# Kernel optimization log

Hardware: AMD Instinct MI355X
Metric: run time of the kernel (lower is better)

## Reference

```python
import jax, jax.numpy as jnp
import numpy as np

N_NODES, IN_DIM, HID, LAT, N_EDGES = 50000, 3000, 512, 30, 800000
NEG_SLOPE = 0.2


def setup_inputs() -> dict:
    key = jax.random.key(0)
    ks = jax.random.split(key, 6)
    x = jax.random.normal(ks[0], (N_NODES, IN_DIM), dtype=jnp.float32)
    edge_index = jax.random.randint(ks[1], (2, N_EDGES), 0, N_NODES, dtype=jnp.int64)
    # xavier-normal-ish scales
    W1 = jax.random.normal(ks[2], (IN_DIM, HID), dtype=jnp.float32) * 0.02
    W2 = jax.random.normal(ks[3], (HID, LAT), dtype=jnp.float32) * 0.06
    att_src = jax.random.normal(ks[4], (HID,), dtype=jnp.float32) * 0.1
    att_dst = jax.random.normal(ks[5], (HID,), dtype=jnp.float32) * 0.1
    return {"x": x, "edge_index": edge_index, "W1": W1, "W2": W2,
            "att_src": att_src, "att_dst": att_dst}


def _segment_softmax(e, seg, num_segments):
    # numerically stable softmax over variable-degree dst neighborhoods
    m = jax.ops.segment_max(e, seg, num_segments=num_segments)
    m = jnp.where(jnp.isfinite(m), m, 0.0)  # empty segments -> 0, harmless
    p = jnp.exp(e - m[seg])
    s = jax.ops.segment_sum(p, seg, num_segments=num_segments)
    return p / (s[seg] + 1e-16)


def reference(x, edge_index, W1, W2, att_src, att_dst):
    N = x.shape[0]
    src, dst = edge_index[0], edge_index[1]  # messages flow src(j) -> dst(i)

    # ---- conv1: full GAT layer (heads=1, no self-loops, no bias) ----
    h1 = x @ W1                                   # [N, 512]
    a_src = h1 @ att_src                          # [N]
    a_dst = h1 @ att_dst                          # [N]
    e = jax.nn.leaky_relu(a_src[src] + a_dst[dst], NEG_SLOPE)  # [E]
    alpha = _segment_softmax(e, dst, N)           # [E] (also tied attn for conv3)
    agg1 = jax.ops.segment_sum(h1[src] * alpha[:, None], dst, num_segments=N)
    x1 = jax.nn.elu(agg1)                         # [N, 512]

    # ---- conv2: attention=False -> plain linear projection ----
    x2 = x1 @ W2                                  # [N, 30] (latent embedding)

    # ---- conv3: tied weights (W2^T) + tied attention from conv1 ----
    h3 = x2 @ W2.T                                # [N, 512]
    agg3 = jax.ops.segment_sum(h3[src] * alpha[:, None], dst, num_segments=N)
    x3 = jax.nn.elu(agg3)

    # ---- conv4: attention=False, tied weights (W1^T) ----
    x4 = x3 @ W1.T                                # [N, in_channels]
    return (x2, x4)
```

## Files before the change

kernel.cpp:

```cpp
#include <hip/hip_runtime.h>

#define N_NODES 50000
#define IN_DIM  3000
#define HID     512
#define LAT     30
#define N_EDGES 800000
#define M_PAD   50048
#define M_PAD2  50176
#define K1_PAD  3008
#define N4_PAD  3072

typedef __bf16 bf16;
typedef unsigned int uint;
typedef __attribute__((ext_vector_type(4))) float f32x4;
typedef __attribute__((ext_vector_type(8))) bf16 bf16x8;

__device__ __forceinline__ float bf2f(bf16 b){ return (float)b; }

__device__ __forceinline__ void gl16(const void* g, void* l){
  __builtin_amdgcn_global_load_lds(
      (const __attribute__((address_space(1))) void*)g,
      (__attribute__((address_space(3))) void*)l, 16, 0, 0);
}

__device__ __forceinline__ int xcd_swz(int orig, int nwg){
  int q = nwg >> 3, r = nwg & 7;
  int xcd = orig & 7, lid = orig >> 3;
  return (xcd < r ? xcd*(q+1) : r*(q+1) + (xcd-r)*q) + lid;
}

__global__ void k_w1t(const float* __restrict__ W1, bf16* __restrict__ W1T){
  int k = blockIdx.x*256 + threadIdx.x;
  int n = blockIdx.y;
  if (k >= K1_PAD) return;
  float v = (k < IN_DIM) ? W1[(long)k*HID + n] : 0.f;
  int kt = k >> 5, c = (k >> 3) & 3, off = k & 7;
  int p = c ^ ((n >> 1) & 3);
  W1T[(long)n*K1_PAD + kt*32 + p*8 + off] = (bf16)v;
}
__global__ void k_w1p(const float* __restrict__ W1, bf16* __restrict__ W1P){
  int k = blockIdx.x*256 + threadIdx.x;
  int n = blockIdx.y;
  if (k >= HID) return;
  float v = (n < IN_DIM) ? W1[(long)n*HID + k] : 0.f;
  int kt = k >> 5, c = (k >> 3) & 3, off = k & 7;
  int p = c ^ ((n >> 1) & 3);
  W1P[(long)n*HID + kt*32 + p*8 + off] = (bf16)v;
}
__global__ void k_w2t(const float* __restrict__ W2, bf16* __restrict__ W2T){
  int k = blockIdx.x*256 + threadIdx.x;
  int n = blockIdx.y;
  if (k >= HID) return;
  float v = (n < LAT) ? W2[(long)k*LAT + n] : 0.f;
  W2T[(long)n*HID + k] = (bf16)v;
}
__global__ void k_w2p(const float* __restrict__ W2, bf16* __restrict__ W2P){
  int t = blockIdx.x*256 + threadIdx.x;
  if (t >= HID*32) return;
  int n = t >> 5, k = t & 31;
  W2P[t] = (bf16)((k < LAT) ? W2[(long)n*LAT + k] : 0.f);
}

__global__ __launch_bounds__(256) void k_cvt(const float* __restrict__ x, bf16* __restrict__ xb){
  int chunk = blockIdx.x*256 + threadIdx.x;
  int row = blockIdx.y;
  if (chunk >= K1_PAD/8) return;
  int c8 = chunk*8;
  bf16x8 o;
  if (row < N_NODES && c8 + 8 <= IN_DIM){
    float4 v0 = *(const float4*)(x + (long)row*IN_DIM + c8);
    float4 v1 = *(const float4*)(x + (long)row*IN_DIM + c8 + 4);
    o[0]=(bf16)v0.x; o[1]=(bf16)v0.y; o[2]=(bf16)v0.z; o[3]=(bf16)v0.w;
    o[4]=(bf16)v1.x; o[5]=(bf16)v1.y; o[6]=(bf16)v1.z; o[7]=(bf16)v1.w;
  } else {
    #pragma unroll
    for (int j=0;j<8;j++){
      int c = c8 + j;
      float v = (row < N_NODES && c < IN_DIM) ? x[(long)row*IN_DIM + c] : 0.f;
      o[j] = (bf16)v;
    }
  }
  *(bf16x8*)(xb + (long)row*K1_PAD + c8) = o;
}

template<bool C_F32>
__global__ __launch_bounds__(512, 2) void gemm2(
    const bf16* __restrict__ A, const bf16* __restrict__ B, void* __restrict__ Cp,
    int lda, int ldb, int KS, int Mvalid, int Nvalid, int ldc, int NBX)
{
  __shared__ bf16 Alds[2][256*32];
  __shared__ bf16 Blds[2][256*32];
  const int tid  = threadIdx.x;
  const int lane = tid & 63;
  const int w    = tid >> 6;
  const int wm   = (w >> 2) * 128;
  const int wn   = (w & 3) * 64;
  const int wgid = xcd_swz(blockIdx.x, gridDim.x);
  const int col0 = (wgid % NBX) * 256, row0 = (wgid / NBX) * 256;

  f32x4 acc[8][4];
  #pragma unroll
  for (int mi=0;mi<8;mi++)
    #pragma unroll
    for (int ni=0;ni<4;ni++)
      acc[mi][ni] = (f32x4){0.f,0.f,0.f,0.f};

  const int srow = tid >> 2;
  const int acl  = (((tid & 3) ^ ((tid >> 3) & 3))) * 8;
  const long a0 = (long)(row0 +       srow) * lda;
  const long a1 = (long)(row0 + 128 + srow) * lda;
  const long b0 = (long)(col0 +       srow) * ldb + (tid & 3) * 8;
  const long b1 = (long)(col0 + 128 + srow) * ldb + (tid & 3) * 8;

#define STG2(buf, ks) do{                                               \
    const int kb_ = (ks) * 32;                                          \
    char* la_ = (char*)&Alds[buf][0] + tid*16;                          \
    char* lb_ = (char*)&Blds[buf][0] + tid*16;                          \
    gl16(A + a0 + kb_ + acl, la_);                                      \
    gl16(A + a1 + kb_ + acl, la_ + 8192);                               \
    gl16(B + b0 + kb_, lb_);                                            \
    gl16(B + b1 + kb_, lb_ + 8192);                                     \
  }while(0)

  STG2(0, 0);

  const int rl = lane & 15;
  const int g  = lane >> 4;
  const int ph = (g ^ ((rl >> 1) & 3)) * 16;

  for (int ks = 0; ks < KS; ks++){
    const int cur = ks & 1;
    if (ks + 1 < KS){
      STG2(cur^1, ks+1);
      asm volatile("s_waitcnt vmcnt(4)" ::: "memory");
    } else {
      asm volatile("s_waitcnt vmcnt(0)" ::: "memory");
    }
    __builtin_amdgcn_s_barrier();

    const char* Ac = (const char*)&Alds[cur][0] + (wm + rl)*64 + ph;
    const char* Bc = (const char*)&Blds[cur][0] + (wn + rl)*64 + ph;
    bf16x8 afr[8], bfr[4];
    #pragma unroll
    for (int mi=0;mi<8;mi++) afr[mi] = *(const bf16x8*)(Ac + mi*1024);
    #pragma unroll
    for (int ni=0;ni<4;ni++) bfr[ni] = *(const bf16x8*)(Bc + ni*1024);
    #pragma unroll
    for (int mi=0;mi<8;mi++)
      #pragma unroll
      for (int ni=0;ni<4;ni++)
        acc[mi][ni] = __builtin_amdgcn_mfma_f32_16x16x32_bf16(afr[mi], bfr[ni], acc[mi][ni], 0, 0, 0);

    __builtin_amdgcn_s_barrier();
  }
#undef STG2

  const int crb  = (lane >> 4) * 4;
  const int ccol = lane & 15;
  #pragma unroll
  for (int mi=0;mi<8;mi++){
    #pragma unroll
    for (int v=0;v<4;v++){
      int r = row0 + wm + mi*16 + crb + v;
      if (r >= Mvalid) continue;
      #pragma unroll
      for (int ni=0;ni<4;ni++){
        int c = col0 + wn + ni*16 + ccol;
        if (c >= Nvalid) continue;
        float val = acc[mi][ni][v];
        if (C_F32) ((float*)Cp)[(long)r*ldc + c] = val;
        else       ((bf16*)Cp)[(long)r*ldc + c] = (bf16)val;
      }
    }
  }
}

template<bool C_F32, bool ELU>
__global__ __launch_bounds__(256) void gemm_glds(
    const bf16* __restrict__ A, const bf16* __restrict__ B, void* __restrict__ Cp,
    int lda, int ldb, int Ksteps, int Mvalid, int Nvalid, int ldc, int NBX)
{
  __shared__ bf16 Alds[2][128*32];
  __shared__ bf16 Blds[2][128*32];
  const int tid  = threadIdx.x;
  const int lane = tid & 63;
  const int w    = tid >> 6;
  const int wm   = (w >> 1) * 64, wn = (w & 1) * 64;
  const int wgid = xcd_swz(blockIdx.x, gridDim.x);
  const int col0 = (wgid % NBX) * 128, row0 = (wgid / NBX) * 128;

  f32x4 acc[4][4];
  #pragma unroll
  for (int mi=0;mi<4;mi++)
    #pragma unroll
    for (int ni=0;ni<4;ni++)
      acc[mi][ni] = (f32x4){0.f,0.f,0.f,0.f};

  const int sr = tid >> 2;
  const int sc = (tid & 3) * 16;
  const char* ga = (const char*)(A + (long)(row0 + sr) * lda) + sc;
  const char* gb = (const char*)(B + (long)(col0 + sr) * ldb) + sc;
  const long astep = (long)64 * lda * 2;
  const long bstep = (long)64 * ldb * 2;

#define STAGE_G(buf, ks) do{                                            \
    const long ko_ = (long)(ks) * 64;                                   \
    char* la_ = (char*)&Alds[buf][0] + sr*64 + sc;                      \
    char* lb_ = (char*)&Blds[buf][0] + sr*64 + sc;                      \
    gl16(ga + ko_,         la_);                                        \
    gl16(ga + ko_ + astep, la_ + 64*64);                                \
    gl16(gb + ko_,         lb_);                                        \
    gl16(gb + ko_ + bstep, lb_ + 64*64);                                \
  }while(0)

  STAGE_G(0, 0);

  for (int ks = 0; ks < Ksteps; ks++){
    const int cur = ks & 1;
    if (ks + 1 < Ksteps){
      STAGE_G(cur^1, ks+1);
      asm volatile("s_waitcnt vmcnt(4)" ::: "memory");
    } else {
      asm volatile("s_waitcnt vmcnt(0)" ::: "memory");
    }
    __builtin_amdgcn_s_barrier();

    const bf16* Ac = &Alds[cur][0];
    const bf16* Bc = &Blds[cur][0];
    bf16x8 af[4], bfr[4];
    #pragma unroll
    for (int mi=0;mi<4;mi++)
      af[mi] = *(const bf16x8*)&Ac[(wm + mi*16 + (lane & 15))*32 + (lane>>4)*8];
    #pragma unroll
    for (int ni=0;ni<4;ni++)
      bfr[ni] = *(const bf16x8*)&Bc[(wn + ni*16 + (lane & 15))*32 + (lane>>4)*8];
    #pragma unroll
    for (int mi=0;mi<4;mi++)
      #pragma unroll
      for (int ni=0;ni<4;ni++)
        acc[mi][ni] = __builtin_amdgcn_mfma_f32_16x16x32_bf16(af[mi], bfr[ni], acc[mi][ni], 0, 0, 0);

    __builtin_amdgcn_s_barrier();
  }
#undef STAGE_G

  const int crb  = (lane >> 4) * 4;
  const int ccol = lane & 15;
  #pragma unroll
  for (int mi=0;mi<4;mi++){
    #pragma unroll
    for (int v=0;v<4;v++){
      int r = row0 + wm + mi*16 + crb + v;
      if (r >= Mvalid) continue;
      #pragma unroll
      for (int ni=0;ni<4;ni++){
        int c = col0 + wn + ni*16 + ccol;
        if (c >= Nvalid) continue;
        float val = acc[mi][ni][v];
        if (ELU) val = (val > 0.f) ? val : expm1f(val);
        if (C_F32) ((float*)Cp)[(long)r*ldc + c] = val;
        else       ((bf16*)Cp)[(long)r*ldc + c] = (bf16)val;
      }
    }
  }
}

__global__ void k_attdots(const bf16* __restrict__ h1, const float* __restrict__ att_s,
                          const float* __restrict__ att_d, float* __restrict__ a_src,
                          float* __restrict__ a_dst){
  int gid = blockIdx.x * blockDim.x + threadIdx.x;
  int row = gid >> 6, lane = gid & 63;
  if (row >= N_NODES) return;
  bf16x8 hv = *(const bf16x8*)(h1 + (long)row*HID + lane*8);
  float s1 = 0.f, s2 = 0.f;
  #pragma unroll
  for (int j=0;j<8;j++){
    float h = bf2f(hv[j]);
    s1 = fmaf(h, att_s[lane*8+j], s1);
    s2 = fmaf(h, att_d[lane*8+j], s2);
  }
  #pragma unroll
  for (int o=32;o>0;o>>=1){ s1 += __shfl_down(s1,o); s2 += __shfl_down(s2,o); }
  if (lane == 0){ a_src[row] = s1; a_dst[row] = s2; }
}

__global__ void k_deg(const int* __restrict__ ei, int* __restrict__ deg){
  int e = blockIdx.x*256 + threadIdx.x;
  if (e >= N_EDGES) return;
  atomicAdd(&deg[ei[N_EDGES + e]], 1);
}

__global__ void k_scan(const int* __restrict__ deg, int* __restrict__ off, int* __restrict__ cur){
  const int n = M_PAD, T = 1024;
  int t = threadIdx.x;
  const int per = (n + T - 1) / T;
  int s0 = t*per, s1 = min(n, s0+per);
  int sum = 0;
  for (int i=s0;i<s1;i++) sum += deg[i];
  __shared__ int sd[1024];
  sd[t] = sum; __syncthreads();
  for (int o=1;o<T;o<<=1){
    int x = (t>=o) ? sd[t-o] : 0;
    __syncthreads();
    sd[t] += x;
    __syncthreads();
  }
  int run = sd[t] - sum;
  for (int i=s0;i<s1;i++){
    off[i] = run; cur[i] = run;
    run += deg[i];
  }
  if (s0 < n && s1 == n) off[n] = run;
}

__global__ void k_fill(const int* __restrict__ ei, int* __restrict__ cur,
                       int* __restrict__ csr_src, const float* __restrict__ a_s,
                       const float* __restrict__ a_d, float* __restrict__ p_e){
  int e = blockIdx.x*256 + threadIdx.x;
  if (e >= N_EDGES) return;
  int s = ei[e];
  int d = ei[N_EDGES + e];
  int pos = atomicAdd(&cur[d], 1);
  csr_src[pos] = s;
  float v = a_s[s] + a_d[d];
  v = (v > 0.f) ? v : 0.2f*v;
  p_e[pos] = __expf(v);
}

__global__ __launch_bounds__(256) void k_agg1w(
    const int* __restrict__ off, const int* __restrict__ csr_src,
    const float* __restrict__ p_edge,
    const bf16* __restrict__ h1, bf16* __restrict__ x1,
    float* __restrict__ s_node)
{
  const int i = blockIdx.x*4 + (threadIdx.x >> 6);
  const int lane = threadIdx.x & 63;
  if (i >= N_NODES) return;
  const int start = off[i];
  const int deg = off[i+1] - start;

  float acc[8];
  #pragma unroll
  for (int j=0;j<8;j++) acc[j] = 0.f;
  float ssum = 0.f;

  for (int k=0;k<deg;k++){
    int s = csr_src[start+k];
    float pk = p_edge[start+k];
    ssum += pk;
    bf16x8 hv = *(const bf16x8*)(h1 + (long)s*HID + lane*8);
    #pragma unroll
    for (int j=0;j<8;j++) acc[j] = fmaf(pk, bf2f(hv[j]), acc[j]);
  }
  float inv = 1.f/(ssum + 1e-16f);
  bf16x8 o;
  #pragma unroll
  for (int j=0;j<8;j++){
    float v = acc[j]*inv;
    v = (v > 0.f) ? v : expm1f(v);
    o[j] = (bf16)v;
  }
  *(bf16x8*)(x1 + (long)i*HID + lane*8) = o;
  if (lane == 0) s_node[i] = ssum;
}

__global__ void k_agg3(const int* __restrict__ off, const int* __restrict__ csr_src,
                       const float* __restrict__ p_edge, const float* __restrict__ s_node,
                       const float* __restrict__ x2, bf16* __restrict__ aggb)
{
  int i = blockIdx.x*8 + (threadIdx.x >> 5);
  int lane = threadIdx.x & 31;
  if (i >= M_PAD2) return;
  float acc = 0.f;
  if (i < N_NODES){
    int s0 = off[i], d = off[i+1] - s0;
    for (int k=0;k<d;k++){
      int s = csr_src[s0+k];
      float pk = p_edge[s0+k];
      if (lane < LAT) acc = fmaf(pk, x2[(long)s*LAT + lane], acc);
    }
    acc *= 1.f/(s_node[i] + 1e-16f);
  }
  aggb[(long)i*32 + lane] = (bf16)((lane < LAT) ? acc : 0.f);
}

extern "C" void kernel_launch(void* const* d_in, const int* in_sizes, int n_in,
                              void* d_out, int out_size, void* d_ws, size_t ws_size,
                              hipStream_t stream)
{
  const float* x     = (const float*)d_in[0];
  const int*   ei    = (const int*)d_in[1];
  const float* W1    = (const float*)d_in[2];
  const float* W2    = (const float*)d_in[3];
  const float* att_s = (const float*)d_in[4];
  const float* att_d = (const float*)d_in[5];

  float* out_x2 = (float*)d_out;
  float* out_x4 = (float*)d_out + (long)N_NODES*LAT;

  bf16* xb = (bf16*)out_x4;
  bf16* h1 = xb + (long)M_PAD2*K1_PAD;
  bf16* x1 = h1 + (long)M_PAD*HID;

  char* w = (char*)d_ws;
  bf16* W1T = (bf16*)w;  w += (long)HID*K1_PAD*2;
  bf16* W1P = (bf16*)w;  w += (long)N4_PAD*HID*2;
  bf16* W2T = (bf16*)w;  w += (long)128*HID*2;
  bf16* W2P = (bf16*)w;  w += (long)HID*32*2;
  bf16* x3  = (bf16*)w;  w += (long)M_PAD2*HID*2;
  bf16* aggb= (bf16*)w;  w += (long)M_PAD2*32*2;
  int* deg  = (int*)w;   w += (long)M_PAD*4;
  int* offs = (int*)w;   w += (long)(M_PAD+64)*4;
  int* cur  = (int*)w;   w += (long)M_PAD*4;
  int* csr  = (int*)w;   w += (long)N_EDGES*4;
  float* p_e = (float*)w; w += (long)N_EDGES*4;
  float* s_n = (float*)w; w += (long)M_PAD*4;
  float* a_s = (float*)w; w += (long)M_PAD*4;
  float* a_d = (float*)w; w += (long)M_PAD*4;

  k_w1t<<<dim3((K1_PAD+255)/256, HID), 256, 0, stream>>>(W1, W1T);
  k_w1p<<<dim3((HID+255)/256, N4_PAD), 256, 0, stream>>>(W1, W1P);
  k_w2t<<<dim3(2, 128), 256, 0, stream>>>(W2, W2T);
  k_w2p<<<(HID*32+255)/256, 256, 0, stream>>>(W2, W2P);
  k_cvt<<<dim3((K1_PAD/8+255)/256, M_PAD2), 256, 0, stream>>>(x, xb);

  hipMemsetAsync(deg, 0, (size_t)M_PAD*4, stream);
  k_deg<<<(N_EDGES+255)/256, 256, 0, stream>>>(ei, deg);
  k_scan<<<1, 1024, 0, stream>>>(deg, offs, cur);

  gemm2<false><<<(HID/256)*(M_PAD2/256), 512, 0, stream>>>(
      xb, W1T, h1, K1_PAD, K1_PAD, K1_PAD/32, N_NODES, HID, HID, HID/256);

  k_attdots<<<(N_NODES*64)/256, 256, 0, stream>>>(h1, att_s, att_d, a_s, a_d);

  k_fill<<<(N_EDGES+255)/256, 256, 0, stream>>>(ei, cur, csr, a_s, a_d, p_e);

  k_agg1w<<<(N_NODES+3)/4, 256, 0, stream>>>(offs, csr, p_e, h1, x1, s_n);

  gemm_glds<true,false><<<1*(M_PAD/128), 256, 0, stream>>>(
      x1, W2T, out_x2, HID, HID, HID/32, N_NODES, LAT, LAT, 1);

  k_agg3<<<(M_PAD2+7)/8, 256, 0, stream>>>(offs, csr, p_e, s_n, out_x2, aggb);
  gemm_glds<false,true><<<(HID/128)*(M_PAD2/128), 256, 0, stream>>>(
      aggb, W2P, x3, 32, 32, 1, M_PAD2, HID, HID, HID/128);

  gemm2<true><<<(N4_PAD/256)*(M_PAD2/256), 512, 0, stream>>>(
      x3, W1P, out_x4, HID, HID, HID/32, N_NODES, IN_DIM, IN_DIM, N4_PAD/256);
}
```

Measured before the change: 1.190 ms.

## Fuse GAT aggregations with the small LAT projections and drop the padded-row conversion

The conv1 aggregation kernel now applies ELU and immediately projects each node row onto W2 through per-wave dot products and shuffle reductions. It writes x2 directly, so the bf16 x1 intermediate and one small GEMM launch go away. The conv3 aggregation likewise computes the 30-wide aggregate and expands it through W2^T with ELU in-register, writing x3 directly and replacing the aggb buffer and its GEMM. The input conversion now covers only real rows and zero-fills the column tail, so padding rows of xb and x3 are left uninitialised; those rows only feed outputs that are never stored. The trade-off is a heavy shuffle reduction (30 values across 6 steps) and redundant per-lane weight reads in place of MFMA-based GEMMs.

```diff
diff --git a/kernel.cpp b/kernel.cpp
--- a/kernel.cpp
+++ b/kernel.cpp
@@ -67,18 +67,14 @@
   if (chunk >= K1_PAD/8) return;
   int c8 = chunk*8;
   bf16x8 o;
-  if (row < N_NODES && c8 + 8 <= IN_DIM){
+  if (c8 + 8 <= IN_DIM){
     float4 v0 = *(const float4*)(x + (long)row*IN_DIM + c8);
     float4 v1 = *(const float4*)(x + (long)row*IN_DIM + c8 + 4);
     o[0]=(bf16)v0.x; o[1]=(bf16)v0.y; o[2]=(bf16)v0.z; o[3]=(bf16)v0.w;
     o[4]=(bf16)v1.x; o[5]=(bf16)v1.y; o[6]=(bf16)v1.z; o[7]=(bf16)v1.w;
   } else {
     #pragma unroll
-    for (int j=0;j<8;j++){
-      int c = c8 + j;
-      float v = (row < N_NODES && c < IN_DIM) ? x[(long)row*IN_DIM + c] : 0.f;
-      o[j] = (bf16)v;
-    }
+    for (int j=0;j<8;j++) o[j] = (bf16)0.f;
   }
   *(bf16x8*)(xb + (long)row*K1_PAD + c8) = o;
 }
@@ -175,96 +171,6 @@
   }
 }
 
-template<bool C_F32, bool ELU>
-__global__ __launch_bounds__(256) void gemm_glds(
-    const bf16* __restrict__ A, const bf16* __restrict__ B, void* __restrict__ Cp,
-    int lda, int ldb, int Ksteps, int Mvalid, int Nvalid, int ldc, int NBX)
-{
-  __shared__ bf16 Alds[2][128*32];
-  __shared__ bf16 Blds[2][128*32];
-  const int tid  = threadIdx.x;
-  const int lane = tid & 63;
-  const int w    = tid >> 6;
-  const int wm   = (w >> 1) * 64, wn = (w & 1) * 64;
-  const int wgid = xcd_swz(blockIdx.x, gridDim.x);
-  const int col0 = (wgid % NBX) * 128, row0 = (wgid / NBX) * 128;
-
-  f32x4 acc[4][4];
-  #pragma unroll
-  for (int mi=0;mi<4;mi++)
-    #pragma unroll
-    for (int ni=0;ni<4;ni++)
-      acc[mi][ni] = (f32x4){0.f,0.f,0.f,0.f};
-
-  const int sr = tid >> 2;
-  const int sc = (tid & 3) * 16;
-  const char* ga = (const char*)(A + (long)(row0 + sr) * lda) + sc;
-  const char* gb = (const char*)(B + (long)(col0 + sr) * ldb) + sc;
-  const long astep = (long)64 * lda * 2;
-  const long bstep = (long)64 * ldb * 2;
-
-#define STAGE_G(buf, ks) do{                                            \
-    const long ko_ = (long)(ks) * 64;                                   \
-    char* la_ = (char*)&Alds[buf][0] + sr*64 + sc;                      \
-    char* lb_ = (char*)&Blds[buf][0] + sr*64 + sc;                      \
-    gl16(ga + ko_,         la_);                                        \
-    gl16(ga + ko_ + astep, la_ + 64*64);                                \
-    gl16(gb + ko_,         lb_);                                        \
-    gl16(gb + ko_ + bstep, lb_ + 64*64);                                \
-  }while(0)
-
-  STAGE_G(0, 0);
-
-  for (int ks = 0; ks < Ksteps; ks++){
-    const int cur = ks & 1;
-    if (ks + 1 < Ksteps){
-      STAGE_G(cur^1, ks+1);
-      asm volatile("s_waitcnt vmcnt(4)" ::: "memory");
-    } else {
-      asm volatile("s_waitcnt vmcnt(0)" ::: "memory");
-    }
-    __builtin_amdgcn_s_barrier();
-
-    const bf16* Ac = &Alds[cur][0];
-    const bf16* Bc = &Blds[cur][0];
-    bf16x8 af[4], bfr[4];
-    #pragma unroll
-    for (int mi=0;mi<4;mi++)
-      af[mi] = *(const bf16x8*)&Ac[(wm + mi*16 + (lane & 15))*32 + (lane>>4)*8];
-    #pragma unroll
-    for (int ni=0;ni<4;ni++)
-      bfr[ni] = *(const bf16x8*)&Bc[(wn + ni*16 + (lane & 15))*32 + (lane>>4)*8];
-    #pragma unroll
-    for (int mi=0;mi<4;mi++)
-      #pragma unroll
-      for (int ni=0;ni<4;ni++)
-        acc[mi][ni] = __builtin_amdgcn_mfma_f32_16x16x32_bf16(af[mi], bfr[ni], acc[mi][ni], 0, 0, 0);
-
-    __builtin_amdgcn_s_barrier();
-  }
-#undef STAGE_G
-
-  const int crb  = (lane >> 4) * 4;
-  const int ccol = lane & 15;
-  #pragma unroll
-  for (int mi=0;mi<4;mi++){
-    #pragma unroll
-    for (int v=0;v<4;v++){
-      int r = row0 + wm + mi*16 + crb + v;
-      if (r >= Mvalid) continue;
-      #pragma unroll
-      for (int ni=0;ni<4;ni++){
-        int c = col0 + wn + ni*16 + ccol;
-        if (c >= Nvalid) continue;
-        float val = acc[mi][ni][v];
-        if (ELU) val = (val > 0.f) ? val : expm1f(val);
-        if (C_F32) ((float*)Cp)[(long)r*ldc + c] = val;
-        else       ((bf16*)Cp)[(long)r*ldc + c] = (bf16)val;
-      }
-    }
-  }
-}
-
 __global__ void k_attdots(const bf16* __restrict__ h1, const float* __restrict__ att_s,
                           const float* __restrict__ att_d, float* __restrict__ a_src,
                           float* __restrict__ a_dst){
@@ -327,10 +233,10 @@
   p_e[pos] = __expf(v);
 }
 
-__global__ __launch_bounds__(256) void k_agg1w(
+__global__ __launch_bounds__(256) void k_agg1x2(
     const int* __restrict__ off, const int* __restrict__ csr_src,
-    const float* __restrict__ p_edge,
-    const bf16* __restrict__ h1, bf16* __restrict__ x1,
+    const float* __restrict__ p_edge, const bf16* __restrict__ h1,
+    const bf16* __restrict__ W2T, float* __restrict__ x2,
     float* __restrict__ s_node)
 {
   const int i = blockIdx.x*4 + (threadIdx.x >> 6);
@@ -353,35 +259,84 @@
     for (int j=0;j<8;j++) acc[j] = fmaf(pk, bf2f(hv[j]), acc[j]);
   }
   float inv = 1.f/(ssum + 1e-16f);
-  bf16x8 o;
+  float xr[8];
   #pragma unroll
   for (int j=0;j<8;j++){
     float v = acc[j]*inv;
+    xr[j] = (v > 0.f) ? v : expm1f(v);
+  }
+  if (lane == 0) s_node[i] = ssum;
+
+  float part[LAT];
+  #pragma unroll
+  for (int j=0;j<LAT;j++){
+    bf16x8 wv = *(const bf16x8*)(W2T + (long)j*HID + lane*8);
+    float p = 0.f;
+    #pragma unroll
+    for (int k=0;k<8;k++) p = fmaf(xr[k], bf2f(wv[k]), p);
+    part[j] = p;
+  }
+  #pragma unroll
+  for (int o=32;o>0;o>>=1){
+    #pragma unroll
+    for (int j=0;j<LAT;j++) part[j] += __shfl_down(part[j], o);
+  }
+  if (lane == 0){
+    #pragma unroll
+    for (int j=0;j<LAT;j++) x2[(long)i*LAT + j] = part[j];
+  }
+}
+
+__global__ __launch_bounds__(256) void k_agg3x3(
+    const int* __restrict__ off, const int* __restrict__ csr_src,
+    const float* __restrict__ p_edge, const float* __restrict__ s_n,
+    const float* __restrict__ x2, const bf16* __restrict__ W2P,
+    bf16* __restrict__ x3)
+{
+  const int i = blockIdx.x*4 + (threadIdx.x >> 6);
+  const int lane = threadIdx.x & 63;
+  if (i >= N_NODES) return;
+  const int hw = lane >> 5, j = lane & 31;
+
+  float a = 0.f;
+  {
+    int s0 = off[i], d = off[i+1] - s0;
+    if (j < LAT){
+      for (int k=hw; k<d; k+=2){
+        int s = csr_src[s0+k];
+        a = fmaf(p_edge[s0+k], x2[(long)s*LAT + j], a);
+      }
+    }
+  }
+  a += __shfl_xor(a, 32);
+  a *= 1.f/(s_n[i] + 1e-16f);
+
+  float ag[LAT];
+  #pragma unroll
+  for (int q=0;q<LAT;q++) ag[q] = __shfl(a, q);
+
+  const int c0 = lane*8;
+  bf16x8 o;
+  #pragma unroll
+  for (int cc=0;cc<8;cc++){
+    const bf16* wr = W2P + (long)(c0+cc)*32;
+    bf16x8 w0 = *(const bf16x8*)(wr);
+    bf16x8 w1 = *(const bf16x8*)(wr+8);
+    bf16x8 w2 = *(const bf16x8*)(wr+16);
+    bf16x8 w3 = *(const bf16x8*)(wr+24);
+    float v = 0.f;
+    #pragma unroll
+    for (int q=0;q<8;q++) v = fmaf(ag[q],    bf2f(w0[q]), v);
+    #pragma unroll
+    for (int q=0;q<8;q++) v = fmaf(ag[8+q],  bf2f(w1[q]), v);
+    #pragma unroll
+    for (int q=0;q<8;q++) v = fmaf(ag[16+q], bf2f(w2[q]), v);
+    #pragma unroll
+    for (int q=0;q<6;q++) v = fmaf(ag[24+q], bf2f(w3[q]), v);
     v = (v > 0.f) ? v : expm1f(v);
-    o[j] = (bf16)v;
-  }
-  *(bf16x8*)(x1 + (long)i*HID + lane*8) = o;
-  if (lane == 0) s_node[i] = ssum;
-}
-
-__global__ void k_agg3(const int* __restrict__ off, const int* __restrict__ csr_src,
-                       const float* __restrict__ p_edge, const float* __restrict__ s_node,
-                       const float* __restrict__ x2, bf16* __restrict__ aggb)
-{
-  int i = blockIdx.x*8 + (threadIdx.x >> 5);
-  int lane = threadIdx.x & 31;
-  if (i >= M_PAD2) return;
-  float acc = 0.f;
-  if (i < N_NODES){
-    int s0 = off[i], d = off[i+1] - s0;
-    for (int k=0;k<d;k++){
-      int s = csr_src[s0+k];
-      float pk = p_edge[s0+k];
-      if (lane < LAT) acc = fmaf(pk, x2[(long)s*LAT + lane], acc);
-    }
-    acc *= 1.f/(s_node[i] + 1e-16f);
-  }
-  aggb[(long)i*32 + lane] = (bf16)((lane < LAT) ? acc : 0.f);
+    o[cc] = (bf16)v;
+  }
+  *(bf16x8*)(x3 + (long)i*HID + c0) = o;
 }
 
 extern "C" void kernel_launch(void* const* d_in, const int* in_sizes, int n_in,
@@ -400,7 +355,6 @@
 
   bf16* xb = (bf16*)out_x4;
   bf16* h1 = xb + (long)M_PAD2*K1_PAD;
-  bf16* x1 = h1 + (long)M_PAD*HID;
 
   char* w = (char*)d_ws;
   bf16* W1T = (bf16*)w;  w += (long)HID*K1_PAD*2;
@@ -408,7 +362,6 @@
   bf16* W2T = (bf16*)w;  w += (long)128*HID*2;
   bf16* W2P = (bf16*)w;  w += (long)HID*32*2;
   bf16* x3  = (bf16*)w;  w += (long)M_PAD2*HID*2;
-  bf16* aggb= (bf16*)w;  w += (long)M_PAD2*32*2;
   int* deg  = (int*)w;   w += (long)M_PAD*4;
   int* offs = (int*)w;   w += (long)(M_PAD+64)*4;
   int* cur  = (int*)w;   w += (long)M_PAD*4;
@@ -422,7 +375,7 @@
   k_w1p<<<dim3((HID+255)/256, N4_PAD), 256, 0, stream>>>(W1, W1P);
   k_w2t<<<dim3(2, 128), 256, 0, stream>>>(W2, W2T);
   k_w2p<<<(HID*32+255)/256, 256, 0, stream>>>(W2, W2P);
-  k_cvt<<<dim3((K1_PAD/8+255)/256, M_PAD2), 256, 0, stream>>>(x, xb);
+  k_cvt<<<dim3(2, N_NODES), 256, 0, stream>>>(x, xb);
 
   hipMemsetAsync(deg, 0, (size_t)M_PAD*4, stream);
   k_deg<<<(N_EDGES+255)/256, 256, 0, stream>>>(ei, deg);
@@ -435,14 +388,9 @@
 
   k_fill<<<(N_EDGES+255)/256, 256, 0, stream>>>(ei, cur, csr, a_s, a_d, p_e);
 
-  k_agg1w<<<(N_NODES+3)/4, 256, 0, stream>>>(offs, csr, p_e, h1, x1, s_n);
-
-  gemm_glds<true,false><<<1*(M_PAD/128), 256, 0, stream>>>(
-      x1, W2T, out_x2, HID, HID, HID/32, N_NODES, LAT, LAT, 1);
-
-  k_agg3<<<(M_PAD2+7)/8, 256, 0, stream>>>(offs, csr, p_e, s_n, out_x2, aggb);
-  gemm_glds<false,true><<<(HID/128)*(M_PAD2/128), 256, 0, stream>>>(
-      aggb, W2P, x3, 32, 32, 1, M_PAD2, HID, HID, HID/128);
+  k_agg1x2<<<(N_NODES+3)/4, 256, 0, stream>>>(offs, csr, p_e, h1, W2T, out_x2, s_n);
+
+  k_agg3x3<<<(N_NODES+3)/4, 256, 0, stream>>>(offs, csr, p_e, s_n, out_x2, W2P, x3);
 
   gemm2<true><<<(N4_PAD/256)*(M_PAD2/256), 512, 0, stream>>>(
       x3, W1P, out_x4, HID, HID, HID/32, N_NODES, IN_DIM, IN_DIM, N4_PAD/256);
```

After: 1.542 ms. 1.3x slower.
